# Optimization experiments

Hardware: AMD Instinct MI355X
Metric: run time of the kernel (lower is better)

The kernel has to match this reference:

```python
import jax, jax.numpy as jnp
import numpy as np

DIM = 1024
NUM_HEADS = 16
HEAD_DIM = DIM // NUM_HEADS
SCALE = HEAD_DIM ** -0.5


def setup_inputs() -> dict:
    key = jax.random.key(0)
    ks = jax.random.split(key, 7)
    B, N, L, C = 2, 1024, 4096, DIM
    s = C ** -0.5
    return {
        "x": jax.random.normal(ks[0], (B, N, C), jnp.float32),
        "y": jax.random.normal(ks[1], (B, L, C), jnp.float32),
        "Wq": jax.random.normal(ks[2], (C, C), jnp.float32) * s,
        "Wk": jax.random.normal(ks[3], (C, C), jnp.float32) * s,
        "Wv": jax.random.normal(ks[4], (C, C), jnp.float32) * s,
        "Wp": jax.random.normal(ks[5], (C, C), jnp.float32) * s,
        "bp": jax.random.normal(ks[6], (C,), jnp.float32) * 0.01,
    }


def reference(x, y, Wq, Wk, Wv, Wp, bp):
    B, N, C = x.shape
    L = y.shape[1]
    H, D = NUM_HEADS, HEAD_DIM
    # torch nn.Linear: out = inp @ W.T
    q = (x @ Wq.T).reshape(B, N, H, D)
    k = (y @ Wk.T).reshape(B, L, H, D)
    v = (y @ Wv.T).reshape(B, L, H, D)
    attn = jnp.einsum("bnhd,blhd->bhnl", q, k)  # [B,H,N,L]
    attn = jax.nn.softmax(SCALE * attn, axis=-1)
    out = jnp.einsum("bhnl,blhd->bnhd", attn, v).reshape(B, N, C)
    return out @ Wp.T + bp
```

## Files before the change

### kernel.cpp

```cpp
#include <hip/hip_runtime.h>
#include <hip/hip_bf16.h>
#include <stdint.h>

typedef __bf16 bf16x8 __attribute__((ext_vector_type(8)));
typedef __bf16 bf16x4 __attribute__((ext_vector_type(4)));
typedef float f32x4 __attribute__((ext_vector_type(4)));

#define MFMA16(a, b, c) __builtin_amdgcn_mfma_f32_16x16x32_bf16((a), (b), (c), 0, 0, 0)
#define SB() __builtin_amdgcn_sched_barrier(0)

__device__ __forceinline__ ushort f2bf(float f) {
  union { float f; uint32_t u; } a; a.f = f;
  uint32_t u = a.u;
  return (ushort)((u + 0x7fffu + ((u >> 16) & 1u)) >> 16);
}

__device__ __forceinline__ void glds16(const void* g, void* l) {
  __builtin_amdgcn_global_load_lds(
      (const __attribute__((address_space(1))) uint32_t*)g,
      (__attribute__((address_space(3))) uint32_t*)l, 16, 0, 0);
}

__global__ __launch_bounds__(256) void cvt_xy(const float* __restrict__ x,
                                              const float* __restrict__ y,
                                              ushort* __restrict__ xb,
                                              ushort* __restrict__ yb) {
  const int bid = blockIdx.x;
  const float* in;
  ushort* out;
  int i;
  if (bid < 2048) { in = x; out = xb; i = bid * 1024 + threadIdx.x * 4; }
  else            { in = y; out = yb; i = (bid - 2048) * 1024 + threadIdx.x * 4; }
  float4 v = *(const float4*)(in + i);
  ushort4 o;
  o.x = f2bf(v.x); o.y = f2bf(v.y); o.z = f2bf(v.z); o.w = f2bf(v.w);
  *(ushort4*)(out + i) = o;
}

__global__ __launch_bounds__(256) void cvt_w(
    const float* __restrict__ a, const float* __restrict__ b,
    const float* __restrict__ c, const float* __restrict__ d,
    ushort* __restrict__ oa, ushort* __restrict__ ob,
    ushort* __restrict__ oc, ushort* __restrict__ od) {
  const int bid = blockIdx.x;
  const int sel = bid >> 10;
  const int i = (bid & 1023) * 1024 + threadIdx.x * 4;
  const float* in = (sel == 0) ? a : (sel == 1) ? b : (sel == 2) ? c : d;
  ushort* out = (sel == 0) ? oa : (sel == 1) ? ob : (sel == 2) ? oc : od;
  float4 v = *(const float4*)(in + i);
  ushort4 o;
  o.x = f2bf(v.x); o.y = f2bf(v.y); o.z = f2bf(v.z); o.w = f2bf(v.w);
  *(ushort4*)(out + i) = o;
}

template <int EPI, int BM, int BN>
__global__ __launch_bounds__(256) void gemm_bt(
    const ushort* __restrict__ A, const ushort* __restrict__ Bw,
    void* __restrict__ Cout, int K, float scale, const float* __restrict__ bias) {
  constexpr int NN = 1024;
  constexpr int WM = BM / 2, WN = BN / 2;
  constexpr int AM = WM / 16, BNF = WN / 16;
  __shared__ ushort ldsA[2][BM * 32];
  __shared__ ushort ldsB[2][BN * 32];
  __shared__ ushort ldsT[(EPI == 1) ? (4 * 64 * 64) : 8];

  const int tid = threadIdx.x;
  const int w = tid >> 6, l = tid & 63;
  const int wm = w >> 1, wn = w & 1;
  const int m0 = blockIdx.x * BM, n0 = blockIdx.y * BN;

  f32x4 acc[AM][BNF] = {};

  const int srow = l >> 2;
  const int schunk = l & 3;

  auto stage = [&](int buf, int kt) {
#pragma unroll
    for (int r = 0; r < BM / 64; ++r) {
      const int rb = r * 64 + w * 16;
      const int row = rb + srow;
      const int j = schunk ^ ((row >> 1) & 3);
      glds16(A + (size_t)(m0 + row) * K + kt + j * 8, (char*)&ldsA[buf][0] + rb * 64);
    }
#pragma unroll
    for (int r = 0; r < BN / 64; ++r) {
      const int rb = r * 64 + w * 16;
      const int row = rb + srow;
      const int j = schunk ^ ((row >> 1) & 3);
      glds16(Bw + (size_t)(n0 + row) * K + kt + j * 8, (char*)&ldsB[buf][0] + rb * 64);
    }
  };

  const int nt = K / 32;
  stage(0, 0);
  asm volatile("s_waitcnt vmcnt(0)" ::: "memory");
  SB(); __builtin_amdgcn_s_barrier(); SB();

  for (int t = 0; t < nt; ++t) {
    const int buf = t & 1;
    if (t + 1 < nt) stage(buf ^ 1, (t + 1) * 32);
    bf16x8 af[AM], bfr[BNF];
#pragma unroll
    for (int a = 0; a < AM; ++a) {
      const int rt = wm * WM + a * 16 + (l & 15);
      const int j = (l >> 4) ^ ((rt >> 1) & 3);
      af[a] = *(const bf16x8*)((const char*)&ldsA[buf][0] + rt * 64 + j * 16);
    }
#pragma unroll
    for (int bx = 0; bx < BNF; ++bx) {
      const int rt = wn * WN + bx * 16 + (l & 15);
      const int j = (l >> 4) ^ ((rt >> 1) & 3);
      bfr[bx] = *(const bf16x8*)((const char*)&ldsB[buf][0] + rt * 64 + j * 16);
    }
#pragma unroll
    for (int am = 0; am < AM; ++am)
#pragma unroll
      for (int bn = 0; bn < BNF; ++bn)
        acc[am][bn] = MFMA16(af[am], bfr[bn], acc[am][bn]);
    if (t + 1 < nt) {
      asm volatile("s_waitcnt vmcnt(0)" ::: "memory");
      SB(); __builtin_amdgcn_s_barrier(); SB();
    }
  }

  if constexpr (EPI == 0) {
#pragma unroll
    for (int am = 0; am < AM; ++am)
#pragma unroll
      for (int bn = 0; bn < BNF; ++bn)
#pragma unroll
        for (int i = 0; i < 4; ++i) {
          const int row = m0 + wm * WM + am * 16 + (l >> 4) * 4 + i;
          const int col = n0 + wn * WN + bn * 16 + (l & 15);
          ((ushort*)Cout)[(size_t)row * NN + col] = f2bf(acc[am][bn][i] * scale);
        }
  } else if constexpr (EPI == 2) {
#pragma unroll
    for (int am = 0; am < AM; ++am)
#pragma unroll
      for (int bn = 0; bn < BNF; ++bn)
#pragma unroll
        for (int i = 0; i < 4; ++i) {
          const int row = m0 + wm * WM + am * 16 + (l >> 4) * 4 + i;
          const int col = n0 + wn * WN + bn * 16 + (l & 15);
          ((float*)Cout)[(size_t)row * NN + col] = acc[am][bn][i] + bias[col];
        }
  } else {
    ushort* tp = ldsT + w * 4096;
#pragma unroll
    for (int am = 0; am < AM; ++am)
#pragma unroll
      for (int bn = 0; bn < BNF; ++bn)
#pragma unroll
        for (int i = 0; i < 4; ++i) {
          const int ml = am * 16 + (l >> 4) * 4 + i;
          const int cl = bn * 16 + (l & 15);
          tp[cl * 64 + ml] = f2bf(acc[am][bn][i]);
        }
    __syncthreads();
#pragma unroll
    for (int it = 0; it < 8; ++it) {
      const int cl = it * 8 + (l >> 3);
      const int mc = l & 7;
      bf16x8 vv = *(const bf16x8*)(tp + cl * 64 + mc * 8);
      const int gcol = n0 + wn * WN + cl;
      const int gm = m0 + wm * WM + mc * 8;
      const int b = gm >> 12;
      const int l_ = gm & 4095;
      const int h = gcol >> 6, d = gcol & 63;
      *(bf16x8*)((ushort*)Cout + (((size_t)b * 16 + h) * 64 + d) * 4096 + l_) = vv;
    }
  }
}

__global__ __launch_bounds__(256) void attn_fused(
    const ushort* __restrict__ qb, const ushort* __restrict__ kb,
    const ushort* __restrict__ vT, ushort* __restrict__ ao) {
  constexpr int H = 16, D = 64, L = 4096, N = 1024, KB = 128;
  __shared__ ushort ldsK[2][KB * 64];
  __shared__ ushort ldsV[2][64 * KB];

  const int tid = threadIdx.x, w = tid >> 6, l = tid & 63;
  const int wg = blockIdx.x;
  const int v = (wg & 7) * 64 + (wg >> 3);
  const int bh = v >> 4;
  const int n0 = (v & 15) * 64;
  const int b = bh >> 4, h = bh & 15;
  const int hq = l >> 4;

  bf16x8 qf[2];
  {
    const int qrow = n0 + w * 16 + (l & 15);
    const ushort* qp = qb + (((size_t)b * N + qrow) * H + h) * D + hq * 8;
    qf[0] = *(const bf16x8*)qp;
    qf[1] = *(const bf16x8*)(qp + 32);
  }

  f32x4 oacc[4] = {};
  float m_run = -1e30f, l_run = 0.f;

  auto stage = [&](int buf, int l0) {
#pragma unroll
    for (int r = 0; r < 4; ++r) {
      const int rb = (w * 4 + r) * 8;
      const int row = rb + (l >> 3);
      const int j = (l & 7) ^ (row & 7);
      glds16(kb + (((size_t)b * L + l0 + row) * H + h) * D + j * 8,
             (char*)&ldsK[buf][0] + rb * 128);
    }
#pragma unroll
    for (int r = 0; r < 4; ++r) {
      const int rb = (w * 4 + r) * 4;
      const int row = rb + (l >> 4);
      const int j = (l & 15) ^ (row & 15);
      glds16(vT + ((size_t)(b * H + h) * D + row) * L + l0 + j * 8,
             (char*)&ldsV[buf][0] + rb * 256);
    }
  };

  stage(0, 0);

  for (int t = 0; t < L / KB; ++t) {
    const int buf = t & 1;
    if (t < L / KB - 1) {
      stage(buf ^ 1, (t + 1) * KB);
      asm volatile("s_waitcnt vmcnt(8)" ::: "memory");
    } else {
      asm volatile("s_waitcnt vmcnt(0)" ::: "memory");
    }
    SB(); __builtin_amdgcn_s_barrier(); SB();

    f32x4 sacc[8] = {};
#pragma unroll
    for (int c = 0; c < 8; ++c) {
      const int rt = c * 16 + (l & 15);
#pragma unroll
      for (int ks = 0; ks < 2; ++ks) {
        const int j = ks * 4 + hq;
        bf16x8 kf = *(const bf16x8*)((const char*)&ldsK[buf][0] + rt * 128 + ((j ^ (rt & 7)) << 4));
        sacc[c] = MFMA16(kf, qf[ks], sacc[c]);
      }
    }

    float mt = -1e30f;
#pragma unroll
    for (int c = 0; c < 8; ++c)
#pragma unroll
      for (int i = 0; i < 4; ++i) mt = fmaxf(mt, sacc[c][i]);
    mt = fmaxf(mt, __shfl_xor(mt, 16, 64));
    mt = fmaxf(mt, __shfl_xor(mt, 32, 64));
    const float mn = fmaxf(m_run, mt);
    const float corr = __builtin_amdgcn_exp2f(m_run - mn);
    float rs = 0.f;
#pragma unroll
    for (int c = 0; c < 8; ++c)
#pragma unroll
      for (int i = 0; i < 4; ++i) {
        const float p = __builtin_amdgcn_exp2f(sacc[c][i] - mn);
        sacc[c][i] = p;
        rs += p;
      }
    rs += __shfl_xor(rs, 16, 64);
    rs += __shfl_xor(rs, 32, 64);
    l_run = l_run * corr + rs;
    m_run = mn;

    float corrO[4];
#pragma unroll
    for (int i = 0; i < 4; ++i) corrO[i] = __shfl(corr, hq * 4 + i, 64);
#pragma unroll
    for (int c = 0; c < 4; ++c)
#pragma unroll
      for (int i = 0; i < 4; ++i) oacc[c][i] *= corrO[i];

    bf16x8 pf[4];
#pragma unroll
    for (int ks = 0; ks < 4; ++ks)
#pragma unroll
      for (int i = 0; i < 4; ++i) {
        pf[ks][i]     = (__bf16)sacc[2 * ks][i];
        pf[ks][4 + i] = (__bf16)sacc[2 * ks + 1][i];
      }

#pragma unroll
    for (int c = 0; c < 4; ++c) {
      const int rt = c * 16 + (l & 15);
      const char* vrow = (const char*)&ldsV[buf][0] + rt * 256 + ((hq & 1) << 3);
#pragma unroll
      for (int ks = 0; ks < 4; ++ks) {
        const int j0 = ks * 4 + (hq >> 1);
        bf16x4 va = *(const bf16x4*)(vrow + ((j0 ^ (rt & 15)) << 4));
        bf16x4 vb = *(const bf16x4*)(vrow + (((j0 + 2) ^ (rt & 15)) << 4));
        bf16x8 vf = __builtin_shufflevector(va, vb, 0, 1, 2, 3, 4, 5, 6, 7);
        oacc[c] = MFMA16(pf[ks], vf, oacc[c]);
      }
    }
    SB(); __builtin_amdgcn_s_barrier(); SB();
  }

  float lr[4];
#pragma unroll
  for (int i = 0; i < 4; ++i) lr[i] = __shfl(l_run, hq * 4 + i, 64);
#pragma unroll
  for (int c = 0; c < 4; ++c)
#pragma unroll
    for (int i = 0; i < 4; ++i) {
      const int n = n0 + w * 16 + hq * 4 + i;
      const int d = c * 16 + (l & 15);
      ao[(((size_t)b * N + n) * H + h) * D + d] = f2bf(oacc[c][i] / lr[i]);
    }
}

extern "C" void kernel_launch(void* const* d_in, const int* in_sizes, int n_in,
                              void* d_out, int out_size, void* d_ws, size_t ws_size,
                              hipStream_t stream) {
  const float* x  = (const float*)d_in[0];
  const float* y  = (const float*)d_in[1];
  const float* Wq = (const float*)d_in[2];
  const float* Wk = (const float*)d_in[3];
  const float* Wv = (const float*)d_in[4];
  const float* Wp = (const float*)d_in[5];
  const float* bp = (const float*)d_in[6];
  float* out = (float*)d_out;

  const size_t M1 = 1u << 20;
  ushort* wsb = (ushort*)d_ws;
  ushort* xb  = wsb;
  ushort* yb  = wsb + 2 * M1;
  ushort* wqb = wsb + 10 * M1;
  ushort* wkb = wsb + 11 * M1;
  ushort* wvb = wsb + 12 * M1;
  ushort* wpb = wsb + 13 * M1;
  ushort* qbf = wsb + 14 * M1;
  ushort* kbf = wsb + 16 * M1;
  ushort* vtb = wsb + 24 * M1;
  ushort* aob = wsb + 32 * M1;

  cvt_xy<<<10240, 256, 0, stream>>>(x, y, xb, yb);
  cvt_w<<<4096, 256, 0, stream>>>(Wq, Wk, Wv, Wp, wqb, wkb, wvb, wpb);

  const float qscale = 0.125f * 1.4426950408889634f;
  gemm_bt<0, 64, 64><<<dim3(32, 16), 256, 0, stream>>>(xb, wqb, qbf, 1024, qscale, nullptr);
  gemm_bt<0, 128, 128><<<dim3(64, 8), 256, 0, stream>>>(yb, wkb, kbf, 1024, 1.0f, nullptr);
  gemm_bt<1, 128, 128><<<dim3(64, 8), 256, 0, stream>>>(yb, wvb, vtb, 1024, 1.0f, nullptr);

  attn_fused<<<512, 256, 0, stream>>>(qbf, kbf, vtb, aob);

  gemm_bt<2, 64, 64><<<dim3(32, 16), 256, 0, stream>>>(aob, wpb, out, 1024, 1.0f, bp);
}
```

Measured before the change: 262.6 us.

## Permute key order for wide V reads, lazy softmax rescale, MFMA priority

Changes the K tile row swizzle and the order in which key rows map to score columns. Each lane's probability fragment then lines up with a contiguous 16-byte V chunk, so one 128-bit LDS read replaces two 64-bit reads plus a shuffle. Rescaling of the output accumulator is skipped unless some row max grows by more than 8 in the exp2 domain, which removes per-tile multiplies and shuffles but lets intermediate values grow by up to 2^8. s_setprio is raised around the MFMA loops to favour matrix issue across waves.

```diff
diff --git a/kernel.cpp b/kernel.cpp
--- a/kernel.cpp
+++ b/kernel.cpp
@@ -187,10 +187,11 @@
   const int n0 = (v & 15) * 64;
   const int b = bh >> 4, h = bh & 15;
   const int hq = l >> 4;
+  const int m = l & 15;
 
   bf16x8 qf[2];
   {
-    const int qrow = n0 + w * 16 + (l & 15);
+    const int qrow = n0 + w * 16 + m;
     const ushort* qp = qb + (((size_t)b * N + qrow) * H + h) * D + hq * 8;
     qf[0] = *(const bf16x8*)qp;
     qf[1] = *(const bf16x8*)(qp + 32);
@@ -204,7 +205,8 @@
     for (int r = 0; r < 4; ++r) {
       const int rb = (w * 4 + r) * 8;
       const int row = rb + (l >> 3);
-      const int j = (l & 7) ^ (row & 7);
+      const int sk = (row & 3) + 4 * ((row >> 3) & 1);
+      const int j = (l & 7) ^ sk;
       glds16(kb + (((size_t)b * L + l0 + row) * H + h) * D + j * 8,
              (char*)&ldsK[buf][0] + rb * 128);
     }
@@ -219,6 +221,9 @@
   };
 
   stage(0, 0);
+
+  const int rtl = 8 * (m >> 2) + (m & 3);
+  const int skl = (m & 3) + 4 * ((m >> 2) & 1);
 
   for (int t = 0; t < L / KB; ++t) {
     const int buf = t & 1;
@@ -231,16 +236,18 @@
     SB(); __builtin_amdgcn_s_barrier(); SB();
 
     f32x4 sacc[8] = {};
+    __builtin_amdgcn_s_setprio(1);
 #pragma unroll
     for (int c = 0; c < 8; ++c) {
-      const int rt = c * 16 + (l & 15);
+      const int rt = 32 * (c >> 1) + 4 * (c & 1) + rtl;
 #pragma unroll
       for (int ks = 0; ks < 2; ++ks) {
         const int j = ks * 4 + hq;
-        bf16x8 kf = *(const bf16x8*)((const char*)&ldsK[buf][0] + rt * 128 + ((j ^ (rt & 7)) << 4));
+        bf16x8 kf = *(const bf16x8*)((const char*)&ldsK[buf][0] + rt * 128 + ((j ^ skl) << 4));
         sacc[c] = MFMA16(kf, qf[ks], sacc[c]);
       }
     }
+    __builtin_amdgcn_s_setprio(0);
 
     float mt = -1e30f;
 #pragma unroll
@@ -249,29 +256,31 @@
       for (int i = 0; i < 4; ++i) mt = fmaxf(mt, sacc[c][i]);
     mt = fmaxf(mt, __shfl_xor(mt, 16, 64));
     mt = fmaxf(mt, __shfl_xor(mt, 32, 64));
-    const float mn = fmaxf(m_run, mt);
-    const float corr = __builtin_amdgcn_exp2f(m_run - mn);
+    if (!__all(mt <= m_run + 8.f)) {
+      const float mn = fmaxf(m_run, mt);
+      const float corr = __builtin_amdgcn_exp2f(m_run - mn);
+      float corrO[4];
+#pragma unroll
+      for (int i = 0; i < 4; ++i) corrO[i] = __shfl(corr, hq * 4 + i, 64);
+#pragma unroll
+      for (int c = 0; c < 4; ++c)
+#pragma unroll
+        for (int i = 0; i < 4; ++i) oacc[c][i] *= corrO[i];
+      l_run *= corr;
+      m_run = mn;
+    }
     float rs = 0.f;
 #pragma unroll
     for (int c = 0; c < 8; ++c)
 #pragma unroll
       for (int i = 0; i < 4; ++i) {
-        const float p = __builtin_amdgcn_exp2f(sacc[c][i] - mn);
+        const float p = __builtin_amdgcn_exp2f(sacc[c][i] - m_run);
         sacc[c][i] = p;
         rs += p;
       }
     rs += __shfl_xor(rs, 16, 64);
     rs += __shfl_xor(rs, 32, 64);
-    l_run = l_run * corr + rs;
-    m_run = mn;
-
-    float corrO[4];
-#pragma unroll
-    for (int i = 0; i < 4; ++i) corrO[i] = __shfl(corr, hq * 4 + i, 64);
-#pragma unroll
-    for (int c = 0; c < 4; ++c)
-#pragma unroll
-      for (int i = 0; i < 4; ++i) oacc[c][i] *= corrO[i];
+    l_run += rs;
 
     bf16x8 pf[4];
 #pragma unroll
@@ -282,19 +291,18 @@
         pf[ks][4 + i] = (__bf16)sacc[2 * ks + 1][i];
       }
 
+    __builtin_amdgcn_s_setprio(1);
 #pragma unroll
     for (int c = 0; c < 4; ++c) {
-      const int rt = c * 16 + (l & 15);
-      const char* vrow = (const char*)&ldsV[buf][0] + rt * 256 + ((hq & 1) << 3);
+      const int rt = c * 16 + m;
 #pragma unroll
       for (int ks = 0; ks < 4; ++ks) {
-        const int j0 = ks * 4 + (hq >> 1);
-        bf16x4 va = *(const bf16x4*)(vrow + ((j0 ^ (rt & 15)) << 4));
-        bf16x4 vb = *(const bf16x4*)(vrow + (((j0 + 2) ^ (rt & 15)) << 4));
-        bf16x8 vf = __builtin_shufflevector(va, vb, 0, 1, 2, 3, 4, 5, 6, 7);
+        const int j = ks * 4 + hq;
+        bf16x8 vf = *(const bf16x8*)((const char*)&ldsV[buf][0] + rt * 256 + ((j ^ (rt & 15)) << 4));
         oacc[c] = MFMA16(pf[ks], vf, oacc[c]);
       }
     }
+    __builtin_amdgcn_s_setprio(0);
     SB(); __builtin_amdgcn_s_barrier(); SB();
   }
 
@@ -306,7 +314,7 @@
 #pragma unroll
     for (int i = 0; i < 4; ++i) {
       const int n = n0 + w * 16 + hq * 4 + i;
-      const int d = c * 16 + (l & 15);
+      const int d = c * 16 + m;
       ao[(((size_t)b * N + n) * H + h) * D + d] = f2bf(oacc[c][i] / lr[i]);
     }
 }
```

Measured after the change: 250.0 us. 1.05x faster.
